# Optimization experiments

Hardware: AMD Instinct MI355X
Metric: run time of the kernel (lower is better)

The kernel has to match this reference:

```python
import jax, jax.numpy as jnp
import numpy as np

B, C, H, W = 8, 512, 32, 32
N_HEADS, HEAD_DIM = 8, 64
EPS = 1e-5


def _layernorm(x, g, b):
    mu = jnp.mean(x, axis=-1, keepdims=True)
    var = jnp.mean(jnp.square(x - mu), axis=-1, keepdims=True)
    return (x - mu) * jax.lax.rsqrt(var + EPS) * g + b


def setup_inputs() -> dict:
    key = jax.random.key(0)
    ks = jax.random.split(key, 16)
    u = lambda k, shp: jax.random.uniform(k, shp, dtype=jnp.float32)
    inp = {
        "x": jax.random.normal(ks[0], (B, C, H, W), dtype=jnp.float32),
        "t": jax.random.normal(ks[1], (B,), dtype=jnp.float32),
        # attention params (torch.rand init in source)
        "K_W": u(ks[2], (N_HEADS, C, HEAD_DIM)), "K_b": u(ks[3], (N_HEADS, HEAD_DIM)),
        "Q_W": u(ks[4], (N_HEADS, C, HEAD_DIM)), "Q_b": u(ks[5], (N_HEADS, HEAD_DIM)),
        "V_W": u(ks[6], (N_HEADS, C, HEAD_DIM)), "V_b": u(ks[7], (N_HEADS, HEAD_DIM)),
        "O_W": u(ks[8], (N_HEADS, HEAD_DIM, C)), "O_b": u(ks[9], (C,)),
        # pre-attention LayerNorm
        "ln1_g": jnp.ones((C,), jnp.float32), "ln1_b": jnp.zeros((C,), jnp.float32),
        # MLP: LayerNorm -> Linear -> GELU -> Linear
        "ln2_g": jnp.ones((C,), jnp.float32), "ln2_b": jnp.zeros((C,), jnp.float32),
        "W1": jax.random.normal(ks[10], (C, C), dtype=jnp.float32) / np.sqrt(C),
        "b1": jnp.zeros((C,), jnp.float32),
        "W2": jax.random.normal(ks[11], (C, C), dtype=jnp.float32) / np.sqrt(C),
        "b2": jnp.zeros((C,), jnp.float32),
    }
    return inp


def reference(x, t, K_W, K_b, Q_W, Q_b, V_W, V_b, O_W, O_b,
              ln1_g, ln1_b, ln2_g, ln2_b, W1, b1, W2, b2):
    b, c, h, w = x.shape
    xs = x.reshape(b, c, h * w).transpose(0, 2, 1)           # b s c
    res = _layernorm(xs, ln1_g, ln1_b)
    q = jnp.einsum('bsc,ncd->bsnd', res, Q_W) + Q_b          # b s n_h h_dim
    k = jnp.einsum('bsc,ncd->bsnd', res, K_W) + K_b
    v = jnp.einsum('bsc,ncd->bsnd', res, V_W) + V_b
    scores = jnp.einsum('bsnd,btnd->bnst', q, k) / jnp.sqrt(jnp.float32(c))
    attn = jax.nn.softmax(scores, axis=-1)                   # b n_h s s
    o = jnp.einsum('bnst,btnd->bsnd', attn, v)
    out = jnp.einsum('bsnd,ndc->bsc', o, O_W) + O_b
    out = out + xs                                           # residual
    m = _layernorm(out, ln2_g, ln2_b)
    m = jax.nn.gelu(m @ W1 + b1, approximate=False) @ W2 + b2
    out = m + out
    return out.transpose(0, 2, 1).reshape(b, c, h, w)
```

## Files before the change

kernel.cpp:

```cpp
#include <hip/hip_runtime.h>
#include <math.h>

#define BB 8
#define CC 512
#define SS 1024
#define NHH 8
#define HDD 64
#define KD 512

typedef __attribute__((ext_vector_type(8))) short short8;
typedef __attribute__((ext_vector_type(4))) float f32x4;
typedef __attribute__((ext_vector_type(4))) unsigned short ushort4v;

__device__ __forceinline__ unsigned short f2bf(float x) {
  union { float f; unsigned int u; } c; c.f = x;
  unsigned int r = (c.u + 0x7FFFu + ((c.u >> 16) & 1u)) >> 16;
  return (unsigned short)r;
}
__device__ __forceinline__ float b2f(unsigned short h) {
  union { unsigned int u; float f; } c; c.u = ((unsigned int)h) << 16; return c.f;
}

#define GLD_LDS(gp, lp) __builtin_amdgcn_global_load_lds( \
    (const __attribute__((address_space(1))) void*)(gp),  \
    (__attribute__((address_space(3))) void*)(lp), 16, 0, 0)

__device__ __forceinline__ float block_reduce_sum(float v) {
  __shared__ float sm[4];
  #pragma unroll
  for (int o = 32; o > 0; o >>= 1) v += __shfl_down(v, o, 64);
  if ((threadIdx.x & 63) == 0) sm[threadIdx.x >> 6] = v;
  __syncthreads();
  float r = (sm[0] + sm[1]) + (sm[2] + sm[3]);
  __syncthreads();
  return r;
}

__global__ __launch_bounds__(256) void ln1_stats(const float* __restrict__ x,
                                                 float2* __restrict__ mustd) {
  const int b = blockIdx.y, s0 = blockIdx.x * 64;
  const int sl = threadIdx.x & 63, cg = threadIdx.x >> 6;
  const float* xp = x + (size_t)b * CC * SS + s0 + sl;
  float ps = 0.f, pq = 0.f;
  #pragma unroll 8
  for (int i = 0; i < 128; ++i) {
    const float v = xp[(size_t)(cg * 128 + i) * SS];
    ps += v; pq += v * v;
  }
  __shared__ float sred[2][4][64];
  sred[0][cg][sl] = ps; sred[1][cg][sl] = pq;
  __syncthreads();
  if (cg == 0) {
    const float s = (sred[0][0][sl] + sred[0][1][sl]) + (sred[0][2][sl] + sred[0][3][sl]);
    const float q = (sred[1][0][sl] + sred[1][1][sl]) + (sred[1][2][sl] + sred[1][3][sl]);
    const float mu = s * (1.0f / CC);
    const float rs = rsqrtf(q * (1.0f / CC) - mu * mu + 1e-5f);
    mustd[b * SS + s0 + sl] = make_float2(mu, rs);
  }
}

__global__ __launch_bounds__(256) void ln1_apply(
    const float* __restrict__ x, const float2* __restrict__ mustd,
    const float* __restrict__ g, const float* __restrict__ be,
    unsigned short* __restrict__ yh, unsigned short* __restrict__ yl,
    unsigned short* __restrict__ xh, unsigned short* __restrict__ xl) {
  __shared__ float tile[32][33];
  const int b = blockIdx.z, c0 = blockIdx.y * 32, s0 = blockIdx.x * 32;
  const int tx = threadIdx.x, ty = threadIdx.y;
  const float* xb = x + ((size_t)b * CC + c0) * SS + s0;
  #pragma unroll
  for (int i = ty; i < 32; i += 8)
    tile[i][tx] = xb[(size_t)i * SS + tx];
  __syncthreads();
  const float gc = g[c0 + tx], bc = be[c0 + tx];
  #pragma unroll
  for (int i = ty; i < 32; i += 8) {
    const float2 ms = mustd[b * SS + s0 + i];
    const float v = tile[tx][i];
    const float y = (v - ms.x) * ms.y * gc + bc;
    const size_t oi = ((size_t)b * SS + s0 + i) * CC + c0 + tx;
    const unsigned short hy = f2bf(y);
    yh[oi] = hy; yl[oi] = f2bf(y - b2f(hy));
    const unsigned short hx = f2bf(v);
    xh[oi] = hx; xl[oi] = f2bf(v - b2f(hx));
  }
}

__global__ __launch_bounds__(256) void ln_bf16_k(const float* __restrict__ in,
                                                 const float* __restrict__ g,
                                                 const float* __restrict__ be,
                                                 unsigned short* __restrict__ outh) {
  size_t row = blockIdx.x;
  const float* r = in + row * CC;
  int t = threadIdx.x;
  float v0 = r[t], v1 = r[t + 256];
  float s = block_reduce_sum(v0 + v1);
  float mu = s * (1.0f / CC);
  float d0 = v0 - mu, d1 = v1 - mu;
  float vs = block_reduce_sum(d0 * d0 + d1 * d1);
  float rstd = rsqrtf(vs * (1.0f / CC) + 1e-5f);
  outh[row * CC + t]       = f2bf(d0 * rstd * g[t] + be[t]);
  outh[row * CC + t + 256] = f2bf(d1 * rstd * g[t + 256] + be[t + 256]);
}

__global__ __launch_bounds__(256) void convert_weights(
    const float* __restrict__ QW, const float* __restrict__ KW,
    const float* __restrict__ VW, const float* __restrict__ OW,
    const float* __restrict__ W1, const float* __restrict__ W2,
    const float* __restrict__ Qb, const float* __restrict__ Kb,
    const float* __restrict__ Vb,
    unsigned short* __restrict__ BtQKh, unsigned short* __restrict__ BtQKl,
    unsigned short* __restrict__ BtVh,
    unsigned short* __restrict__ BtOh, unsigned short* __restrict__ BtOl,
    unsigned short* __restrict__ BtW1h, unsigned short* __restrict__ BtW2h,
    float* __restrict__ qkvb) {
  const float SCL = 0.044194173824159216f * 1.4426950408889634f;
  __shared__ float tile[32][33];
  const int p = blockIdx.z, wsel = p >> 3, sub = p & 7;
  const int k0 = blockIdx.x * 32, d0 = blockIdx.y * 32;
  const int tx = threadIdx.x, ty = threadIdx.y;
  const float* w; int rs; unsigned short *dh, *dl; int nbase; float mul = 1.0f;
  switch (wsel) {
    case 0:  w = QW + sub * 32768; rs = 64;  dh = BtQKh; dl = BtQKl;  nbase = sub * 64; mul = SCL; break;
    case 1:  w = KW + sub * 32768; rs = 64;  dh = BtQKh; dl = BtQKl;  nbase = 512 + sub * 64;  break;
    case 2:  w = VW + sub * 32768; rs = 64;  dh = BtVh;  dl = nullptr; nbase = sub * 64;       break;
    case 3:  w = OW + sub * 64;    rs = 512; dh = BtOh;  dl = BtOl;   nbase = sub * 64;        break;
    case 4:  w = W1 + sub * 64;    rs = 512; dh = BtW1h; dl = nullptr; nbase = sub * 64;       break;
    default: w = W2 + sub * 64;    rs = 512; dh = BtW2h; dl = nullptr; nbase = sub * 64;       break;
  }
  for (int i = ty; i < 32; i += 8)
    tile[i][tx] = w[(size_t)(k0 + i) * rs + d0 + tx];
  __syncthreads();
  for (int i = ty; i < 32; i += 8) {
    float f = tile[tx][i] * mul;
    unsigned short h = f2bf(f);
    size_t idx = (size_t)(nbase + d0 + i) * KD + k0 + tx;
    dh[idx] = h;
    if (dl) dl[idx] = f2bf(f - b2f(h));
  }
  if (p == 0 && blockIdx.x == 0 && blockIdx.y == 0) {
    int t = ty * 32 + tx;
    for (int i = t; i < 1536; i += 256)
      qkvb[i] = i < 512 ? Qb[i] * SCL : (i < 1024 ? Kb[i - 512] : Vb[i - 1024]);
  }
}

__global__ __launch_bounds__(256) void gemm_qkv(
    const unsigned short* __restrict__ Ah, const unsigned short* __restrict__ Al,
    const unsigned short* __restrict__ Bth, const unsigned short* __restrict__ Btl,
    const float* __restrict__ bias,
    unsigned short* __restrict__ qkh, unsigned short* __restrict__ qkl,
    unsigned short* __restrict__ vt) {
  __shared__ __align__(16) unsigned short smem[4 * 128 * 32];
  unsigned short* As = smem;
  unsigned short* Bs = smem + 2 * 128 * 32;
  const int tid = threadIdx.x;
  const int w = tid >> 6, l = tid & 63, quad = l >> 4, lm = l & 15;
  const int f = blockIdx.x, xcd = f & 7, gidx = f >> 3;
  const int n0 = (gidx >> 3) * 128;
  const int m0 = (((gidx & 7) << 3) | xcd) * 128;
  const bool splitB = n0 < 1024;
  const int wm = (w >> 1) * 64, wn = (w & 1) * 64;
  const int srow = tid >> 2;
  const int sch = (((tid & 3) ^ (srow & 3)) * 8);
  const unsigned short* Agh = Ah + (size_t)(m0 + srow) * KD + sch;
  const unsigned short* Agl = Al + (size_t)(m0 + srow) * KD + sch;
  const unsigned short* Bgh = Bth + (size_t)(n0 + srow) * KD + sch;
  const unsigned short* Bgl = Btl + (size_t)(n0 + srow) * KD + sch;
  unsigned short* Aswh = As + w * 512;
  unsigned short* Aswl = As + 4096 + w * 512;
  unsigned short* Bswh = Bs + w * 512;
  unsigned short* Bswl = Bs + 4096 + w * 512;
  const int rch = ((quad ^ (lm & 3)) * 8);
  const f32x4 fzero = {0.f, 0.f, 0.f, 0.f};
  f32x4 acc[4][4];
  #pragma unroll
  for (int i = 0; i < 4; ++i)
    #pragma unroll
    for (int j = 0; j < 4; ++j) acc[i][j] = fzero;
  for (int k0 = 0; k0 < KD; k0 += 32) {
    __syncthreads();
    GLD_LDS(Agh + k0, Aswh);
    GLD_LDS(Agh + k0 + 64 * KD, Aswh + 2048);
    GLD_LDS(Agl + k0, Aswl);
    GLD_LDS(Agl + k0 + 64 * KD, Aswl + 2048);
    GLD_LDS(Bgh + k0, Bswh);
    GLD_LDS(Bgh + k0 + 64 * KD, Bswh + 2048);
    if (splitB) {
      GLD_LDS(Bgl + k0, Bswl);
      GLD_LDS(Bgl + k0 + 64 * KD, Bswl + 2048);
    }
    __syncthreads();
    short8 afh[4], afl[4], bfh[4], bfl[4];
    #pragma unroll
    for (int i = 0; i < 4; ++i) {
      afh[i] = *(const short8*)(As + (wm + i * 16 + lm) * 32 + rch);
      afl[i] = *(const short8*)(As + 4096 + (wm + i * 16 + lm) * 32 + rch);
    }
    #pragma unroll
    for (int j = 0; j < 4; ++j)
      bfh[j] = *(const short8*)(Bs + (wn + j * 16 + lm) * 32 + rch);
    if (splitB) {
      #pragma unroll
      for (int j = 0; j < 4; ++j)
        bfl[j] = *(const short8*)(Bs + 4096 + (wn + j * 16 + lm) * 32 + rch);
      #pragma unroll
      for (int i = 0; i < 4; ++i)
        #pragma unroll
        for (int j = 0; j < 4; ++j) {
          f32x4 t = acc[i][j];
          t = __builtin_amdgcn_mfma_f32_16x16x32_bf16(afh[i], bfh[j], t, 0, 0, 0);
          t = __builtin_amdgcn_mfma_f32_16x16x32_bf16(afh[i], bfl[j], t, 0, 0, 0);
          t = __builtin_amdgcn_mfma_f32_16x16x32_bf16(afl[i], bfh[j], t, 0, 0, 0);
          acc[i][j] = t;
        }
    } else {
      #pragma unroll
      for (int i = 0; i < 4; ++i)
        #pragma unroll
        for (int j = 0; j < 4; ++j)
          acc[i][j] = __builtin_amdgcn_mfma_f32_16x16x32_bf16(afh[i], bfh[j], acc[i][j], 0, 0, 0);
    }
  }
  if (splitB) {
    #pragma unroll
    for (int i = 0; i < 4; ++i) {
      const int row = m0 + wm + i * 16 + quad * 4;
      #pragma unroll
      for (int j = 0; j < 4; ++j) {
        const int ncol = n0 + wn + j * 16 + lm;
        const float bv = bias[ncol];
        #pragma unroll
        for (int r = 0; r < 4; ++r) {
          const float xv = acc[i][j][r] + bv;
          const size_t oi = (size_t)(row + r) * 1024 + ncol;
          unsigned short h = f2bf(xv);
          qkh[oi] = h;
          qkl[oi] = f2bf(xv - b2f(h));
        }
      }
    }
  } else {
    __syncthreads();
    #pragma unroll
    for (int i = 0; i < 4; ++i) {
      const int mlb = wm + i * 16 + quad * 4;
      #pragma unroll
      for (int j = 0; j < 4; ++j) {
        const int nl = wn + j * 16 + lm;
        const float bv = bias[n0 + nl];
        ushort4v pk;
        #pragma unroll
        for (int r = 0; r < 4; ++r) pk[r] = f2bf(acc[i][j][r] + bv);
        const int chunk = ((mlb >> 3) ^ (nl & 15));
        *(ushort4v*)(smem + nl * 128 + chunk * 8 + (mlb & 7)) = pk;
      }
    }
    __syncthreads();
    const int tn = tid >> 4, tc = tid & 15;
    const int bb2 = m0 >> 10, sbase = m0 & 1023;
    #pragma unroll
    for (int pass = 0; pass < 8; ++pass) {
      const int nl = pass * 16 + tn;
      const int hh = (n0 - 1024 + nl) >> 6, dd = nl & 63;
      short8 v8 = *(const short8*)(smem + nl * 128 + ((tc ^ (nl & 15)) * 8));
      *(short8*)(vt + ((size_t)(bb2 * 8 + hh) * 64 + dd) * 1024 + sbase + tc * 8) = v8;
    }
  }
}

template<int SB, int GELU, int OUTMODE, int RESID, int TRANS>
__global__ __launch_bounds__(256) void gemm64(
    const unsigned short* __restrict__ Ah,
    const unsigned short* __restrict__ Bh, const unsigned short* __restrict__ Bl,
    const float* __restrict__ bias, const float* __restrict__ residf,
    const unsigned short* __restrict__ residh, const unsigned short* __restrict__ residl,
    unsigned short* __restrict__ outh, float* __restrict__ outf, int ldc) {
  constexpr int STAGE = (SB ? 3 : 2) * 8192;
  constexpr int TSIZE = TRANS ? 64 * 65 * 4 : 0;
  __shared__ __align__(16) unsigned char smem[STAGE > TSIZE ? STAGE : TSIZE];
  unsigned short* As  = (unsigned short*)smem;
  unsigned short* Bs  = (unsigned short*)(smem + 8192);
  unsigned short* Bls = (unsigned short*)(smem + 16384);
  float (*ttile)[65]  = (float(*)[65])smem;
  const int tid = threadIdx.x;
  const int w = tid >> 6, l = tid & 63, quad = l >> 4, lm = l & 15;
  const int f = blockIdx.x, xcd = f & 7, gidx = f >> 3;
  const int n0 = (gidx >> 4) * 64;
  const int m0 = (((gidx & 15) << 3) | xcd) * 64;
  const int wm = (w >> 1) * 32, wn = (w & 1) * 32;
  const int srow8 = tid >> 3;
  const int sch8  = ((tid & 7) ^ (srow8 & 7)) * 8;
  const unsigned short* Ag  = Ah + (size_t)(m0 + srow8) * KD + sch8;
  const unsigned short* Bg  = Bh + (size_t)(n0 + srow8) * KD + sch8;
  const unsigned short* Bgl = SB ? Bl + (size_t)(n0 + srow8) * KD + sch8 : nullptr;
  const f32x4 fzero = {0.f, 0.f, 0.f, 0.f};
  f32x4 acc[2][2];
  #pragma unroll
  for (int i = 0; i < 2; ++i)
    #pragma unroll
    for (int j = 0; j < 2; ++j) acc[i][j] = fzero;
  for (int k0 = 0; k0 < KD; k0 += 64) {
    __syncthreads();
    GLD_LDS(Ag + k0, As + w * 512);
    GLD_LDS(Ag + k0 + 32 * KD, As + 2048 + w * 512);
    GLD_LDS(Bg + k0, Bs + w * 512);
    GLD_LDS(Bg + k0 + 32 * KD, Bs + 2048 + w * 512);
    if constexpr (SB) {
      GLD_LDS(Bgl + k0, Bls + w * 512);
      GLD_LDS(Bgl + k0 + 32 * KD, Bls + 2048 + w * 512);
    }
    __syncthreads();
    #pragma unroll
    for (int ks = 0; ks < 2; ++ks) {
      const int kc = ((ks * 4 + quad) ^ (lm & 7)) * 8;
      short8 af[2], bfh[2], bfl[2];
      #pragma unroll
      for (int i = 0; i < 2; ++i)
        af[i] = *(const short8*)(As + (wm + i * 16 + lm) * 64 + kc);
      #pragma unroll
      for (int j = 0; j < 2; ++j)
        bfh[j] = *(const short8*)(Bs + (wn + j * 16 + lm) * 64 + kc);
      if constexpr (SB) {
        #pragma unroll
        for (int j = 0; j < 2; ++j)
          bfl[j] = *(const short8*)(Bls + (wn + j * 16 + lm) * 64 + kc);
      }
      #pragma unroll
      for (int i = 0; i < 2; ++i)
        #pragma unroll
        for (int j = 0; j < 2; ++j) {
          f32x4 t = acc[i][j];
          t = __builtin_amdgcn_mfma_f32_16x16x32_bf16(af[i], bfh[j], t, 0, 0, 0);
          if constexpr (SB)
            t = __builtin_amdgcn_mfma_f32_16x16x32_bf16(af[i], bfl[j], t, 0, 0, 0);
          acc[i][j] = t;
        }
    }
  }
  if constexpr (TRANS) __syncthreads();
  #pragma unroll
  for (int i = 0; i < 2; ++i) {
    const int row = m0 + wm + i * 16 + quad * 4;
    #pragma unroll
    for (int j = 0; j < 2; ++j) {
      const int col = n0 + wn + j * 16 + lm;
      const float bv = bias[col];
      #pragma unroll
      for (int r = 0; r < 4; ++r) {
        float x = acc[i][j][r] + bv;
        if (GELU) x = 0.5f * x * (1.0f + erff(x * 0.70710678118654752f));
        const size_t ri = (size_t)(row + r) * CC + col;
        if (RESID == 1) x += residf[ri];
        if (RESID == 2) x += b2f(residh[ri]) + b2f(residl[ri]);
        if constexpr (TRANS) {
          ttile[wm + i * 16 + quad * 4 + r][wn + j * 16 + lm] = x;
        } else {
          const size_t oi = (size_t)(row + r) * ldc + col;
          if (OUTMODE == 0) outf[oi] = x;
          else outh[oi] = f2bf(x);
        }
      }
    }
  }
  if constexpr (TRANS) {
    __syncthreads();
    const int bi = m0 >> 10, s0 = m0 & 1023;
    const int s = tid & 63;
    #pragma unroll
    for (int c0 = 0; c0 < 64; c0 += 4) {
      const int col = c0 + (tid >> 6);
      outf[(size_t)(bi * 512 + n0 + col) * 1024 + s0 + s] = ttile[s][col];
    }
  }
}

__global__ __launch_bounds__(256) void attn_mfma(
    const unsigned short* __restrict__ QKh, const unsigned short* __restrict__ QKl,
    const unsigned short* __restrict__ Vt, unsigned short* __restrict__ Oh) {
  __shared__ __align__(16) unsigned short Ksh[64 * 64], Ksl[64 * 64];
  __shared__ __align__(16) unsigned short Vts[64 * 64];
  __shared__ __align__(16) unsigned short Ps[4 * 16 * 88];
  const int f = blockIdx.x, xcd = f & 7, gidx = f >> 3;
  const int bh = (xcd << 3) | (gidx >> 4);
  const int q0 = (gidx & 15) * 64, h = bh & 7, b = bh >> 3;
  const int tid = threadIdx.x, w = tid >> 6, l = tid & 63, quad = l >> 4, lm = l & 15;
  const int LDQ = 2 * CC;
  const size_t qkbase = (size_t)b * SS * LDQ;
  const int srow8 = tid >> 3;
  const int sch8  = ((tid & 7) ^ (srow8 & 7)) * 8;
  const unsigned short* Vg = Vt + ((size_t)(b * 8 + h) * 64 + srow8) * 1024 + sch8;
  short8 qh[2], ql[2];
  {
    const size_t qo = qkbase + (size_t)(q0 + w * 16 + lm) * LDQ + h * 64 + quad * 8;
    qh[0] = *(const short8*)(QKh + qo);
    qh[1] = *(const short8*)(QKh + qo + 32);
    ql[0] = *(const short8*)(QKl + qo);
    ql[1] = *(const short8*)(QKl + qo + 32);
  }
  short8 bones;
  #pragma unroll
  for (int u = 0; u < 8; ++u) bones[u] = (lm == 0) ? (short)0x3F80 : (short)0;
  const f32x4 fzero = {0.f, 0.f, 0.f, 0.f};
  float mrow[4];
  f32x4 oacc[5];
  #pragma unroll
  for (int r = 0; r < 4; ++r) mrow[r] = -1e30f;
  #pragma unroll
  for (int j = 0; j < 5; ++j) oacc[j] = fzero;
  unsigned short* Pw = Ps + w * (16 * 88);
  for (int kt = 0; kt < SS; kt += 64) {
    __syncthreads();
    {
      const unsigned short* kg  = QKh + qkbase + (size_t)(kt + srow8) * LDQ + CC + h * 64 + sch8;
      const unsigned short* kgl = QKl + qkbase + (size_t)(kt + srow8) * LDQ + CC + h * 64 + sch8;
      GLD_LDS(kg, Ksh + w * 512);
      GLD_LDS(kg + 32 * LDQ, Ksh + 2048 + w * 512);
      GLD_LDS(kgl, Ksl + w * 512);
      GLD_LDS(kgl + 32 * LDQ, Ksl + 2048 + w * 512);
      GLD_LDS(Vg + kt, Vts + w * 512);
      GLD_LDS(Vg + kt + 32 * 1024, Vts + 2048 + w * 512);
    }
    __syncthreads();
    f32x4 sc[4];
    #pragma unroll
    for (int j = 0; j < 4; ++j) sc[j] = fzero;
    #pragma unroll
    for (int st = 0; st < 2; ++st) {
      const int kc = ((st * 4 + quad) ^ (lm & 7)) * 8;
      #pragma unroll
      for (int j = 0; j < 4; ++j) {
        short8 kh = *(const short8*)(Ksh + (j * 16 + lm) * 64 + kc);
        short8 kl = *(const short8*)(Ksl + (j * 16 + lm) * 64 + kc);
        f32x4 t = sc[j];
        t = __builtin_amdgcn_mfma_f32_16x16x32_bf16(qh[st], kh, t, 0, 0, 0);
        t = __builtin_amdgcn_mfma_f32_16x16x32_bf16(qh[st], kl, t, 0, 0, 0);
        t = __builtin_amdgcn_mfma_f32_16x16x32_bf16(ql[st], kh, t, 0, 0, 0);
        sc[j] = t;
      }
    }
    #pragma unroll
    for (int r = 0; r < 4; ++r) {
      float mt = fmaxf(fmaxf(sc[0][r], sc[1][r]), fmaxf(sc[2][r], sc[3][r]));
      #pragma unroll
      for (int mask = 1; mask < 16; mask <<= 1) mt = fmaxf(mt, __shfl_xor(mt, mask, 64));
      const float mn = fmaxf(mrow[r], mt);
      const float alpha = exp2f(mrow[r] - mn);
      mrow[r] = mn;
      #pragma unroll
      for (int j = 0; j < 4; ++j) sc[j][r] = exp2f(sc[j][r] - mn);
      #pragma unroll
      for (int j = 0; j < 5; ++j) oacc[j][r] *= alpha;
    }
    #pragma unroll
    for (int r = 0; r < 4; ++r)
      #pragma unroll
      for (int j = 0; j < 4; ++j) {
        union { float f; unsigned int u; } pc; pc.f = sc[j][r];
        Pw[(quad * 4 + r) * 88 + j * 16 + lm] = (unsigned short)(pc.u >> 16);
      }
    #pragma unroll
    for (int st = 0; st < 2; ++st) {
      short8 ap = *(const short8*)(Pw + lm * 88 + st * 32 + quad * 8);
      const int kc = ((st * 4 + quad) ^ (lm & 7)) * 8;
      #pragma unroll
      for (int j = 0; j < 4; ++j) {
        short8 vv = *(const short8*)(Vts + (j * 16 + lm) * 64 + kc);
        oacc[j] = __builtin_amdgcn_mfma_f32_16x16x32_bf16(ap, vv, oacc[j], 0, 0, 0);
      }
      oacc[4] = __builtin_amdgcn_mfma_f32_16x16x32_bf16(ap, bones, oacc[4], 0, 0, 0);
    }
  }
  float inv[4];
  #pragma unroll
  for (int r = 0; r < 4; ++r) {
    const float lv = __shfl(oacc[4][r], l & 48, 64);
    inv[r] = 1.f / lv;
  }
  const size_t obase =
      (size_t)b * SS * CC + (size_t)(q0 + w * 16 + quad * 4) * CC + h * 64 + lm;
  #pragma unroll
  for (int j = 0; j < 4; ++j)
    #pragma unroll
    for (int r = 0; r < 4; ++r)
      Oh[obase + (size_t)r * CC + j * 16] = f2bf(oacc[j][r] * inv[r]);
}

extern "C" void kernel_launch(void* const* d_in, const int* in_sizes, int n_in,
                              void* d_out, int out_size, void* d_ws, size_t ws_size,
                              hipStream_t stream) {
  const float* x    = (const float*)d_in[0];
  const float* K_W  = (const float*)d_in[2];
  const float* K_b  = (const float*)d_in[3];
  const float* Q_W  = (const float*)d_in[4];
  const float* Q_b  = (const float*)d_in[5];
  const float* V_W  = (const float*)d_in[6];
  const float* V_b  = (const float*)d_in[7];
  const float* O_W  = (const float*)d_in[8];
  const float* O_b  = (const float*)d_in[9];
  const float* ln1g = (const float*)d_in[10];
  const float* ln1b = (const float*)d_in[11];
  const float* ln2g = (const float*)d_in[12];
  const float* ln2b = (const float*)d_in[13];
  const float* W1   = (const float*)d_in[14];
  const float* b1   = (const float*)d_in[15];
  const float* W2   = (const float*)d_in[16];
  const float* b2   = (const float*)d_in[17];
  float* out = (float*)d_out;

  unsigned char* ws = (unsigned char*)d_ws;
  const size_t MB = 1u << 20;
  unsigned short* qkh   = (unsigned short*)(ws);
  unsigned short* qkl   = (unsigned short*)(ws + 16 * MB);
  unsigned short* vt    = (unsigned short*)(ws + 32 * MB);
  unsigned short* ln1h  = (unsigned short*)(ws + 40 * MB);
  unsigned short* ln1l  = (unsigned short*)(ws + 48 * MB);
  unsigned short* xsh   = (unsigned short*)(ws + 56 * MB);
  unsigned short* xsl   = (unsigned short*)(ws + 64 * MB);
  unsigned short* oh    = ln1h;
  float* out1           = (float*)(ws + 72 * MB);
  unsigned short* ln2h  = qkh;
  unsigned short* geluh = (unsigned short*)(ws + 8 * MB);
  unsigned short* BtAll = (unsigned short*)(ws + 88 * MB);
  unsigned short* BtQKh = BtAll;
  unsigned short* BtVh  = BtAll + 1024 * 512;
  unsigned short* BtQKl = BtVh + 512 * 512;
  unsigned short* BtOh  = BtQKl + 1024 * 512;
  unsigned short* BtOl  = BtOh + 512 * 512;
  unsigned short* BtW1h = BtOl + 512 * 512;
  unsigned short* BtW2h = BtW1h + 512 * 512;
  float* qkvb           = (float*)(BtW2h + 512 * 512);
  float2* mustd         = (float2*)(ws + 96 * MB);

  dim3 tb32(32, 8);
  convert_weights<<<dim3(16, 2, 48), tb32, 0, stream>>>(
      Q_W, K_W, V_W, O_W, W1, W2, Q_b, K_b, V_b,
      BtQKh, BtQKl, BtVh, BtOh, BtOl, BtW1h, BtW2h, qkvb);
  ln1_stats<<<dim3(SS / 64, BB), 256, 0, stream>>>(x, mustd);
  ln1_apply<<<dim3(SS / 32, CC / 32, BB), tb32, 0, stream>>>(
      x, mustd, ln1g, ln1b, ln1h, ln1l, xsh, xsl);
  gemm_qkv<<<768, 256, 0, stream>>>(
      ln1h, ln1l, BtAll, BtQKl, qkvb, qkh, qkl, vt);
  attn_mfma<<<1024, 256, 0, stream>>>(qkh, qkl, vt, oh);
  gemm64<1, 0, 0, 2, 0><<<1024, 256, 0, stream>>>(
      oh, BtOh, BtOl, O_b, nullptr, xsh, xsl, nullptr, out1, CC);
  ln_bf16_k<<<BB * SS, 256, 0, stream>>>(out1, ln2g, ln2b, ln2h);
  gemm64<0, 1, 1, 0, 0><<<1024, 256, 0, stream>>>(
      ln2h, BtW1h, nullptr, b1, nullptr, nullptr, nullptr, geluh, nullptr, CC);
  gemm64<0, 0, 0, 1, 1><<<1024, 256, 0, stream>>>(
      geluh, BtW2h, nullptr, b2, out1, nullptr, nullptr, nullptr, out, CC);
}
```

Before: 285.5 us.

## Fuse weight conversion with LN1 stats; skip unchanged softmax rescale in attention

```diff
diff --git a/kernel.cpp b/kernel.cpp
--- a/kernel.cpp
+++ b/kernel.cpp
@@ -34,29 +34,6 @@
   float r = (sm[0] + sm[1]) + (sm[2] + sm[3]);
   __syncthreads();
   return r;
-}
-
-__global__ __launch_bounds__(256) void ln1_stats(const float* __restrict__ x,
-                                                 float2* __restrict__ mustd) {
-  const int b = blockIdx.y, s0 = blockIdx.x * 64;
-  const int sl = threadIdx.x & 63, cg = threadIdx.x >> 6;
-  const float* xp = x + (size_t)b * CC * SS + s0 + sl;
-  float ps = 0.f, pq = 0.f;
-  #pragma unroll 8
-  for (int i = 0; i < 128; ++i) {
-    const float v = xp[(size_t)(cg * 128 + i) * SS];
-    ps += v; pq += v * v;
-  }
-  __shared__ float sred[2][4][64];
-  sred[0][cg][sl] = ps; sred[1][cg][sl] = pq;
-  __syncthreads();
-  if (cg == 0) {
-    const float s = (sred[0][0][sl] + sred[0][1][sl]) + (sred[0][2][sl] + sred[0][3][sl]);
-    const float q = (sred[1][0][sl] + sred[1][1][sl]) + (sred[1][2][sl] + sred[1][3][sl]);
-    const float mu = s * (1.0f / CC);
-    const float rs = rsqrtf(q * (1.0f / CC) - mu * mu + 1e-5f);
-    mustd[b * SS + s0 + sl] = make_float2(mu, rs);
-  }
 }
 
 __global__ __launch_bounds__(256) void ln1_apply(
@@ -103,7 +80,7 @@
   outh[row * CC + t + 256] = f2bf(d1 * rstd * g[t + 256] + be[t + 256]);
 }
 
-__global__ __launch_bounds__(256) void convert_weights(
+__global__ __launch_bounds__(256) void convert_and_stats(
     const float* __restrict__ QW, const float* __restrict__ KW,
     const float* __restrict__ VW, const float* __restrict__ OW,
     const float* __restrict__ W1, const float* __restrict__ W2,
@@ -113,35 +90,61 @@
     unsigned short* __restrict__ BtVh,
     unsigned short* __restrict__ BtOh, unsigned short* __restrict__ BtOl,
     unsigned short* __restrict__ BtW1h, unsigned short* __restrict__ BtW2h,
-    float* __restrict__ qkvb) {
-  const float SCL = 0.044194173824159216f * 1.4426950408889634f;
-  __shared__ float tile[32][33];
-  const int p = blockIdx.z, wsel = p >> 3, sub = p & 7;
-  const int k0 = blockIdx.x * 32, d0 = blockIdx.y * 32;
-  const int tx = threadIdx.x, ty = threadIdx.y;
-  const float* w; int rs; unsigned short *dh, *dl; int nbase; float mul = 1.0f;
-  switch (wsel) {
-    case 0:  w = QW + sub * 32768; rs = 64;  dh = BtQKh; dl = BtQKl;  nbase = sub * 64; mul = SCL; break;
-    case 1:  w = KW + sub * 32768; rs = 64;  dh = BtQKh; dl = BtQKl;  nbase = 512 + sub * 64;  break;
-    case 2:  w = VW + sub * 32768; rs = 64;  dh = BtVh;  dl = nullptr; nbase = sub * 64;       break;
-    case 3:  w = OW + sub * 64;    rs = 512; dh = BtOh;  dl = BtOl;   nbase = sub * 64;        break;
-    case 4:  w = W1 + sub * 64;    rs = 512; dh = BtW1h; dl = nullptr; nbase = sub * 64;       break;
-    default: w = W2 + sub * 64;    rs = 512; dh = BtW2h; dl = nullptr; nbase = sub * 64;       break;
-  }
-  for (int i = ty; i < 32; i += 8)
-    tile[i][tx] = w[(size_t)(k0 + i) * rs + d0 + tx];
-  __syncthreads();
-  for (int i = ty; i < 32; i += 8) {
-    float f = tile[tx][i] * mul;
-    unsigned short h = f2bf(f);
-    size_t idx = (size_t)(nbase + d0 + i) * KD + k0 + tx;
-    dh[idx] = h;
-    if (dl) dl[idx] = f2bf(f - b2f(h));
-  }
-  if (p == 0 && blockIdx.x == 0 && blockIdx.y == 0) {
-    int t = ty * 32 + tx;
-    for (int i = t; i < 1536; i += 256)
-      qkvb[i] = i < 512 ? Qb[i] * SCL : (i < 1024 ? Kb[i - 512] : Vb[i - 1024]);
+    float* __restrict__ qkvb,
+    const float* __restrict__ x, float2* __restrict__ mustd) {
+  const int bid = blockIdx.x;
+  if (bid < 1536) {
+    const float SCL = 0.044194173824159216f * 1.4426950408889634f;
+    __shared__ float tile[32][33];
+    const int bx = bid & 15, by = (bid >> 4) & 1, p = bid >> 5;
+    const int wsel = p >> 3, sub = p & 7;
+    const int k0 = bx * 32, d0 = by * 32;
+    const int tx = threadIdx.x & 31, ty = threadIdx.x >> 5;
+    const float* w; int rs; unsigned short *dh, *dl; int nbase; float mul = 1.0f;
+    switch (wsel) {
+      case 0:  w = QW + sub * 32768; rs = 64;  dh = BtQKh; dl = BtQKl;  nbase = sub * 64; mul = SCL; break;
+      case 1:  w = KW + sub * 32768; rs = 64;  dh = BtQKh; dl = BtQKl;  nbase = 512 + sub * 64;  break;
+      case 2:  w = VW + sub * 32768; rs = 64;  dh = BtVh;  dl = nullptr; nbase = sub * 64;       break;
+      case 3:  w = OW + sub * 64;    rs = 512; dh = BtOh;  dl = BtOl;   nbase = sub * 64;        break;
+      case 4:  w = W1 + sub * 64;    rs = 512; dh = BtW1h; dl = nullptr; nbase = sub * 64;       break;
+      default: w = W2 + sub * 64;    rs = 512; dh = BtW2h; dl = nullptr; nbase = sub * 64;       break;
+    }
+    for (int i = ty; i < 32; i += 8)
+      tile[i][tx] = w[(size_t)(k0 + i) * rs + d0 + tx];
+    __syncthreads();
+    for (int i = ty; i < 32; i += 8) {
+      float f = tile[tx][i] * mul;
+      unsigned short h = f2bf(f);
+      size_t idx = (size_t)(nbase + d0 + i) * KD + k0 + tx;
+      dh[idx] = h;
+      if (dl) dl[idx] = f2bf(f - b2f(h));
+    }
+    if (bid == 0) {
+      int t = threadIdx.x;
+      for (int i = t; i < 1536; i += 256)
+        qkvb[i] = i < 512 ? Qb[i] * SCL : (i < 1024 ? Kb[i - 512] : Vb[i - 1024]);
+    }
+  } else {
+    const int bid2 = bid - 1536;
+    const int b = bid2 >> 4, s0 = (bid2 & 15) * 64;
+    const int sl = threadIdx.x & 63, cg = threadIdx.x >> 6;
+    const float* xp = x + (size_t)b * CC * SS + s0 + sl;
+    float ps = 0.f, pq = 0.f;
+    #pragma unroll 8
+    for (int i = 0; i < 128; ++i) {
+      const float v = xp[(size_t)(cg * 128 + i) * SS];
+      ps += v; pq += v * v;
+    }
+    __shared__ float sred[2][4][64];
+    sred[0][cg][sl] = ps; sred[1][cg][sl] = pq;
+    __syncthreads();
+    if (cg == 0) {
+      const float s = (sred[0][0][sl] + sred[0][1][sl]) + (sred[0][2][sl] + sred[0][3][sl]);
+      const float q = (sred[1][0][sl] + sred[1][1][sl]) + (sred[1][2][sl] + sred[1][3][sl]);
+      const float mu = s * (1.0f / CC);
+      const float rs = rsqrtf(q * (1.0f / CC) - mu * mu + 1e-5f);
+      mustd[b * SS + s0 + sl] = make_float2(mu, rs);
+    }
   }
 }
 
@@ -423,35 +426,54 @@
     }
     __syncthreads();
     f32x4 sc[4];
-    #pragma unroll
-    for (int j = 0; j < 4; ++j) sc[j] = fzero;
-    #pragma unroll
-    for (int st = 0; st < 2; ++st) {
-      const int kc = ((st * 4 + quad) ^ (lm & 7)) * 8;
+    {
+      const int kc = (quad ^ (lm & 7)) * 8;
+      #pragma unroll
+      for (int j = 0; j < 4; ++j) {
+        short8 kh = *(const short8*)(Ksh + (j * 16 + lm) * 64 + kc);
+        short8 kl = *(const short8*)(Ksl + (j * 16 + lm) * 64 + kc);
+        f32x4 t = __builtin_amdgcn_mfma_f32_16x16x32_bf16(qh[0], kh, fzero, 0, 0, 0);
+        t = __builtin_amdgcn_mfma_f32_16x16x32_bf16(qh[0], kl, t, 0, 0, 0);
+        t = __builtin_amdgcn_mfma_f32_16x16x32_bf16(ql[0], kh, t, 0, 0, 0);
+        sc[j] = t;
+      }
+    }
+    {
+      const int kc = ((4 + quad) ^ (lm & 7)) * 8;
       #pragma unroll
       for (int j = 0; j < 4; ++j) {
         short8 kh = *(const short8*)(Ksh + (j * 16 + lm) * 64 + kc);
         short8 kl = *(const short8*)(Ksl + (j * 16 + lm) * 64 + kc);
         f32x4 t = sc[j];
-        t = __builtin_amdgcn_mfma_f32_16x16x32_bf16(qh[st], kh, t, 0, 0, 0);
-        t = __builtin_amdgcn_mfma_f32_16x16x32_bf16(qh[st], kl, t, 0, 0, 0);
-        t = __builtin_amdgcn_mfma_f32_16x16x32_bf16(ql[st], kh, t, 0, 0, 0);
+        t = __builtin_amdgcn_mfma_f32_16x16x32_bf16(qh[1], kh, t, 0, 0, 0);
+        t = __builtin_amdgcn_mfma_f32_16x16x32_bf16(qh[1], kl, t, 0, 0, 0);
+        t = __builtin_amdgcn_mfma_f32_16x16x32_bf16(ql[1], kh, t, 0, 0, 0);
         sc[j] = t;
       }
     }
+    float mnew[4];
+    bool chg = false;
     #pragma unroll
     for (int r = 0; r < 4; ++r) {
       float mt = fmaxf(fmaxf(sc[0][r], sc[1][r]), fmaxf(sc[2][r], sc[3][r]));
       #pragma unroll
       for (int mask = 1; mask < 16; mask <<= 1) mt = fmaxf(mt, __shfl_xor(mt, mask, 64));
-      const float mn = fmaxf(mrow[r], mt);
-      const float alpha = exp2f(mrow[r] - mn);
-      mrow[r] = mn;
-      #pragma unroll
-      for (int j = 0; j < 4; ++j) sc[j][r] = exp2f(sc[j][r] - mn);
-      #pragma unroll
-      for (int j = 0; j < 5; ++j) oacc[j][r] *= alpha;
-    }
+      mnew[r] = fmaxf(mrow[r], mt);
+      chg = chg || (mnew[r] > mrow[r]);
+    }
+    if (__any(chg)) {
+      #pragma unroll
+      for (int r = 0; r < 4; ++r) {
+        const float alpha = exp2f(mrow[r] - mnew[r]);
+        mrow[r] = mnew[r];
+        #pragma unroll
+        for (int j = 0; j < 5; ++j) oacc[j][r] *= alpha;
+      }
+    }
+    #pragma unroll
+    for (int r = 0; r < 4; ++r)
+      #pragma unroll
+      for (int j = 0; j < 4; ++j) sc[j][r] = exp2f(sc[j][r] - mrow[r]);
     #pragma unroll
     for (int r = 0; r < 4; ++r)
       #pragma unroll
@@ -533,10 +555,9 @@
   float2* mustd         = (float2*)(ws + 96 * MB);
 
   dim3 tb32(32, 8);
-  convert_weights<<<dim3(16, 2, 48), tb32, 0, stream>>>(
+  convert_and_stats<<<1536 + 128, 256, 0, stream>>>(
       Q_W, K_W, V_W, O_W, W1, W2, Q_b, K_b, V_b,
-      BtQKh, BtQKl, BtVh, BtOh, BtOl, BtW1h, BtW2h, qkvb);
-  ln1_stats<<<dim3(SS / 64, BB), 256, 0, stream>>>(x, mustd);
+      BtQKh, BtQKl, BtVh, BtOh, BtOl, BtW1h, BtW2h, qkvb, x, mustd);
   ln1_apply<<<dim3(SS / 32, CC / 32, BB), tb32, 0, stream>>>(
       x, mustd, ln1g, ln1b, ln1h, ln1l, xsh, xsl);
   gemm_qkv<<<768, 256, 0, stream>>>(
```

Result: faster. 269.7 us (-5.5%).
